# Performance work log

Hardware: AMD Instinct MI355X
Metric: run time of the kernel (lower is better)

Reference implementation:

```python
import jax, jax.numpy as jnp
import numpy as np

B, S = 4, 4096
DIM = 256
DF = 128   # dim_fourier = floor(256*0.5)
DS = 128   # dim_spline = 256 - 128
GF = 5     # fourier grid_size
GS = 5     # spline grid_size
K = 3      # spline order
P = 0.5
MIN_FREQ = 1e-6
LN_EPS = 1e-5


def _spline_grid():
    h = 2.0 / GS  # grid_range [-1, 1]
    g = np.arange(-K, GS + K + 1, dtype=np.float32) * h - 1.0
    return jnp.asarray(np.broadcast_to(g, (DS, g.shape[0])).copy())  # (DS, GS+2K+1)


def _base_freq():
    return jnp.asarray((1.0 / 10 ** np.linspace(0, 9, DF, dtype=np.float32)).reshape(DF, 1))


def b_splines(x, grid):
    # x: (N, DS); grid: (DS, GS+2K+1). Recursive de Boor B-spline basis.
    xe = x[:, :, None]
    bases = ((xe >= grid[:, :-1]) & (xe < grid[:, 1:])).astype(x.dtype)  # (N, DS, GS+2K)
    for k in range(1, K + 1):
        left = (xe - grid[:, : -(k + 1)]) / (grid[:, k:-1] - grid[:, : -(k + 1)])
        right = (grid[:, k + 1:] - xe) / (grid[:, k + 1:] - grid[:, 1:-k])
        bases = left * bases[:, :, :-1] + right * bases[:, :, 1:]
    return bases  # (N, DS, GS+K)


def setup_inputs() -> dict:
    key = jax.random.key(0)
    ks = jax.random.split(key, 8)
    timestamps = jax.random.uniform(ks[0], (B, S), dtype=jnp.float32)
    freq_theta = jnp.zeros((DF, 1), dtype=jnp.float32)
    bias_fourier = jnp.zeros((DF,), dtype=jnp.float32)
    fourier_weight = jax.random.normal(ks[1], (2, DF, DF, GF), dtype=jnp.float32) / (
        np.sqrt(DF) * np.sqrt(GF))
    w1_spline_w = jnp.asarray((1.0 / 10 ** np.linspace(0, 9, DS, dtype=np.float32)).reshape(DS, 1))
    w1_spline_b = jnp.zeros((DS,), dtype=jnp.float32)
    base_weight = jax.random.normal(ks[2], (DS, DS), dtype=jnp.float32) / np.sqrt(DS)
    spline_weight = jax.random.normal(ks[3], (DS, DS, GS + K), dtype=jnp.float32) / np.sqrt(DS * (GS + K))
    scale_weight = jnp.ones((DIM,), dtype=jnp.float32)
    ln_weight = jnp.ones((DIM,), dtype=jnp.float32)
    ln_bias = jnp.zeros((DIM,), dtype=jnp.float32)
    return {
        "timestamps": timestamps,
        "freq_theta": freq_theta,
        "bias_fourier": bias_fourier,
        "fourier_weight": fourier_weight,
        "w1_spline_w": w1_spline_w,
        "w1_spline_b": w1_spline_b,
        "base_weight": base_weight,
        "spline_weight": spline_weight,
        "scale_weight": scale_weight,
        "ln_weight": ln_weight,
        "ln_bias": ln_bias,
    }


def reference(timestamps, freq_theta, bias_fourier, fourier_weight,
              w1_spline_w, w1_spline_b, base_weight, spline_weight,
              scale_weight, ln_weight, ln_bias):
    grid = _spline_grid()
    base_freq = _base_freq()
    t = timestamps[..., None]  # (B, S, 1)

    # ---- Fourier branch ----
    freq_scale = jax.nn.softplus(freq_theta) + MIN_FREQ          # (DF, 1)
    freq_weight = base_freq * freq_scale                          # (DF, 1)
    proj_f = t * freq_weight[:, 0] + bias_fourier                 # (B, S, DF)
    xf = proj_f.reshape(-1, DF)                                   # (N, DF)
    kfreq = jnp.arange(1, GF + 1, dtype=xf.dtype)                 # (GF,)
    arg = xf[:, :, None] * kfreq                                  # (N, DF, GF)
    # Same math as torch's broadcast-then-sum, expressed as a contraction:
    # y[n,o] = sum_{d,g} cos(arg)[n,d,g] * Wc[o,d,g] + sin * Ws
    y_f = (jnp.einsum('ndg,odg->no', jnp.cos(arg), fourier_weight[0])
           + jnp.einsum('ndg,odg->no', jnp.sin(arg), fourier_weight[1])
           + fourier_weight[0].dtype.type(0) + jnp.zeros((DF,), xf.dtype))
    y_f = y_f  # bias of FourierSeries is zeros param; include explicitly below
    fourier_bias = jnp.zeros((DF,), xf.dtype)
    y_f = y_f + fourier_bias
    out_fourier = y_f.reshape(B, S, DF)

    # ---- Spline branch ----
    proj_s = t * w1_spline_w[:, 0] + w1_spline_b                  # (B, S, DS)
    xs = proj_s.reshape(-1, DS)                                   # (N, DS)
    base_out = jnp.tanh(xs) @ base_weight.T                       # (N, DS)
    bsp = b_splines(xs, grid).reshape(xs.shape[0], -1)            # (N, DS*(GS+K))
    spline_out = bsp @ spline_weight.reshape(DS, -1).T            # (N, DS)
    out_spline = (base_out + spline_out).reshape(B, S, DS)

    # ---- Combine (padded concat == concat of weighted halves) ----
    out = jnp.concatenate([out_fourier * P, out_spline * (1.0 - P)], axis=-1)  # (B, S, DIM)

    # LayerNorm then learnable scale
    mu = jnp.mean(out, axis=-1, keepdims=True)
    var = jnp.mean((out - mu) ** 2, axis=-1, keepdims=True)
    out = (out - mu) * jax.lax.rsqrt(var + LN_EPS) * ln_weight + ln_bias
    out = out * scale_weight
    return out
```

## Files before the change

kernel.cpp:

```cpp
#include <hip/hip_runtime.h>


typedef __attribute__((ext_vector_type(8))) _Float16 half8;
typedef __attribute__((ext_vector_type(2))) __fp16 fp16x2;
typedef __attribute__((ext_vector_type(16))) float f32x16;

#define KN5 -0.19999998807907104f
#define KN6  0.20000004768371582f
#define KN7  0.60000002384185791f

__device__ __forceinline__ unsigned pk(float a, float b) {
    fp16x2 h = __builtin_amdgcn_cvt_pkrtz(a, b);
    return __builtin_bit_cast(unsigned, h);
}

#define SPL9(x, o0,o1,o2,o3,o4,o5,o6,o7,o8) do {                          \
    float ax_ = fabsf(x);                                                  \
    float e_  = __expf(-2.f*ax_);                                          \
    float th_ = (1.f - e_) * __builtin_amdgcn_rcpf(1.f + e_);              \
    o0 = ((x) < 0.f) ? -th_ : th_;                                         \
    bool b1_ = ((x) >= KN6), b2_ = ((x) >= KN7);                           \
    float kn_ = b2_ ? KN7 : (b1_ ? KN6 : KN5);                             \
    float u_  = ((x) - kn_) * 2.5f;                                        \
    float um_ = 1.f - u_;                                                  \
    float u2_ = u_*u_, u3_ = u2_*u_, um2_ = um_*um_, um3_ = um2_*um_;      \
    float w0_ = (1.f/6.f)*um3_, w3_ = (1.f/6.f)*u3_;                       \
    float w1_ = 0.6666666666666667f - u2_  + 0.5f*u3_;                     \
    float w2_ = 0.6666666666666667f - um2_ + 0.5f*um3_;                    \
    o1 = 0.f; o2 = 0.f;                                                    \
    o3 = b1_ ? 0.f : w0_;                                                  \
    o4 = b2_ ? 0.f : (b1_ ? w0_ : w1_);                                    \
    o5 = b2_ ? w0_ : (b1_ ? w1_ : w2_);                                    \
    o6 = b2_ ? w1_ : (b1_ ? w2_ : w3_);                                    \
    o7 = b2_ ? w2_ : (b1_ ? w3_ : 0.f);                                    \
    o8 = b2_ ? w3_ : 0.f;                                                  \
} while (0)

__global__ __launch_bounds__(256) void prep_kernel(
    const float* __restrict__ FW,
    const float* __restrict__ BW,
    const float* __restrict__ SW,
    _Float16* __restrict__ WFP, _Float16* __restrict__ WSP)
{
    int tt = blockIdx.x * 256 + threadIdx.x;
    if (tt >= 327680) return;
    int e = tt & 7, l = (tt >> 3) & 63, frag = tt >> 9;
    int isS = frag >= 320;
    int f = isS ? frag - 320 : frag;
    int col = (f / 80) * 32 + (l & 31);
    int k = (f % 80) * 16 + (l >> 5) * 8 + e;
    int d = k / 10, j = k - d * 10;
    float val;
    if (!isS) {
        int p = (j >= 5), g = j - p * 5;
        val = FW[p * 81920 + col * 640 + d * 5 + g];
    } else {
        val = (j == 0) ? BW[col * 128 + d]
            : (j <= 8) ? SW[col * 1024 + d * 8 + (j - 1)] : 0.f;
    }
    (isS ? WSP : WFP)[(size_t)(f * 64 + l) * 8 + e] = (_Float16)val;
}

__global__ __launch_bounds__(256) void fused_kernel(
    const float* __restrict__ TS, const float* __restrict__ FTHETA,
    const float* __restrict__ BFOUR, const float* __restrict__ W1W,
    const float* __restrict__ W1B, const float* __restrict__ LNW,
    const float* __restrict__ LNB, const float* __restrict__ SCW,
    const _Float16* __restrict__ WFP, const _Float16* __restrict__ WSP,
    float* __restrict__ OUT)
{
    __shared__ __align__(16) _Float16 feat0[32 * 160];
    __shared__ __align__(16) _Float16 feat1[32 * 160];
    __shared__ float tsS[32], fwS[128], bfS[128], w1wS[128], w1bS[128];
    __shared__ float redS[32][4], redQ[32][4], muS[32], rsS[32];

    const int tid  = threadIdx.x;
    const int lane = tid & 63;
    const int wc   = tid >> 6;
    const int l31  = lane & 31, lh = lane >> 5;
    const int row0 = blockIdx.x * 32;

    if (tid < 32) tsS[tid] = TS[row0 + tid];
    if (tid < 128) {
        int d = tid;
        float th = FTHETA[d];
        float sp = (th > 20.f) ? th : log1pf(__expf(th));
        float ex = (float)((double)d * (9.0 / 127.0));
        fwS[d] = (1.0f / powf(10.f, ex)) * (sp + 1e-6f);
        bfS[d] = BFOUR[d];
    } else {
        int d = tid - 128;
        w1wS[d] = W1W[d];
        w1bS[d] = W1B[d];
    }
    __syncthreads();

    const int dd   = tid & 15;
    const int rowA = tid >> 4, rowB = rowA + 16;
    const float tA = tsS[rowA], tB = tsS[rowB];
    const int bA = rowA * 320 + dd * 20, swA = (rowA & 7) << 4;
    const int bB = rowB * 320 + dd * 20, swB = (rowB & 7) << 4;
    const int abase = l31 * 320, aswz = (l31 & 7) << 4;

    f32x16 acc1 = {};
    f32x16 acc2 = {};

    auto computeFour = [&](int ch, _Float16* buf) {
        int d = ch * 16 + dd;
        float fw = fwS[d], bf = bfS[d];
        char* p = (char*)buf;
#pragma unroll
        for (int q = 0; q < 2; ++q) {
            float base = (q ? tB : tA) * fw + bf;
            int b = q ? bB : bA, sw = q ? swB : swA;
            float s1, c1;
            __sincosf(base, &s1, &c1);
            float tc = c1 + c1;
            float c2 = tc*c1 - 1.f, c3 = tc*c2 - c1, c4 = tc*c3 - c2, c5 = tc*c4 - c3;
            float s2 = tc*s1,       s3 = tc*s2 - s1, s4 = tc*s3 - s2, s5 = tc*s4 - s3;
            *(unsigned*)(p + ((b +  0) ^ sw)) = pk(c1, c2);
            *(unsigned*)(p + ((b +  4) ^ sw)) = pk(c3, c4);
            *(unsigned*)(p + ((b +  8) ^ sw)) = pk(c5, s1);
            *(unsigned*)(p + ((b + 12) ^ sw)) = pk(s2, s3);
            *(unsigned*)(p + ((b + 16) ^ sw)) = pk(s4, s5);
        }
    };

    auto computeSpl = [&](int ch, _Float16* buf) {
        int d = ch * 16 + dd;
        float ww = w1wS[d], wb = w1bS[d];
        char* p = (char*)buf;
#pragma unroll
        for (int q = 0; q < 2; ++q) {
            float x = (q ? tB : tA) * ww + wb;
            int b = q ? bB : bA, sw = q ? swB : swA;
            float t0,b0,b1,b2,b3,b4,b5,b6,b7;
            SPL9(x, t0,b0,b1,b2,b3,b4,b5,b6,b7);
            *(unsigned*)(p + ((b +  0) ^ sw)) = pk(t0, b0);
            *(unsigned*)(p + ((b +  4) ^ sw)) = pk(b1, b2);
            *(unsigned*)(p + ((b +  8) ^ sw)) = pk(b3, b4);
            *(unsigned*)(p + ((b + 12) ^ sw)) = pk(b5, b6);
            *(unsigned*)(p + ((b + 16) ^ sw)) = pk(b7, 0.f);
        }
    };

    auto mfmaF = [&](int ch, const _Float16* buf) {
        const char* p = (const char*)buf;
#pragma unroll
        for (int ks = 0; ks < 10; ++ks) {
            half8 b = *(const half8*)(WFP + (size_t)((wc*80 + ch*10 + ks)*64 + lane) * 8);
            half8 a = *(const half8*)(p + ((abase + ks*32 + lh*16) ^ aswz));
            acc1 = __builtin_amdgcn_mfma_f32_32x32x16_f16(a, b, acc1, 0, 0, 0);
        }
    };

    auto mfmaS = [&](int ch, const _Float16* buf) {
        const char* p = (const char*)buf;
#pragma unroll
        for (int ks = 0; ks < 10; ++ks) {
            half8 b = *(const half8*)(WSP + (size_t)((wc*80 + ch*10 + ks)*64 + lane) * 8);
            half8 a = *(const half8*)(p + ((abase + ks*32 + lh*16) ^ aswz));
            acc2 = __builtin_amdgcn_mfma_f32_32x32x16_f16(a, b, acc2, 0, 0, 0);
        }
    };

    computeFour(0, feat0);
    __syncthreads();
    for (int ph = 0; ph < 16; ++ph) {
        _Float16* nb = ((ph + 1) & 1) ? feat1 : feat0;
        const _Float16* cb = (ph & 1) ? feat1 : feat0;
        int nx = ph + 1;
        if (nx < 8)       computeFour(nx, nb);
        else if (nx < 16) computeSpl(nx - 8, nb);
        if (ph < 8) mfmaF(ph, cb);
        else        mfmaS(ph - 8, cb);
        __syncthreads();
    }

#pragma unroll
    for (int g = 0; g < 16; ++g) {
        float xf = 0.5f * acc1[g];
        float xs = 0.5f * acc2[g];
        float s  = xf + xs;
        float qq = xf*xf + xs*xs;
#pragma unroll
        for (int m = 1; m < 32; m <<= 1) {
            s  += __shfl_xor(s, m);
            qq += __shfl_xor(qq, m);
        }
        if (l31 == 0) {
            int r = (g & 3) + 8*(g >> 2) + 4*lh;
            redS[r][wc] = s;
            redQ[r][wc] = qq;
        }
    }
    __syncthreads();
    if (tid < 32) {
        float s  = redS[tid][0] + redS[tid][1] + redS[tid][2] + redS[tid][3];
        float qq = redQ[tid][0] + redQ[tid][1] + redQ[tid][2] + redQ[tid][3];
        float mu = s * (1.0f / 256.0f);
        float var = qq * (1.0f / 256.0f) - mu * mu;
        muS[tid] = mu;
        rsS[tid] = rsqrtf(var + 1e-5f);
    }
    __syncthreads();
    {
        int cF = wc*32 + l31, cS = cF + 128;
        float gF = LNW[cF]*SCW[cF], hF = LNB[cF]*SCW[cF];
        float gS = LNW[cS]*SCW[cS], hS = LNB[cS]*SCW[cS];
#pragma unroll
        for (int g = 0; g < 16; ++g) {
            int r = (g & 3) + 8*(g >> 2) + 4*lh;
            float mu = muS[r], rr = rsS[r];
            size_t base = (size_t)(row0 + r) * 256;
            OUT[base + cF] = (0.5f*acc1[g] - mu)*rr*gF + hF;
            OUT[base + cS] = (0.5f*acc2[g] - mu)*rr*gS + hS;
        }
    }
}

extern "C" void kernel_launch(void* const* d_in, const int* in_sizes, int n_in,
                              void* d_out, int out_size, void* d_ws, size_t ws_size,
                              hipStream_t stream) {
    const float* TS     = (const float*)d_in[0];
    const float* FTHETA = (const float*)d_in[1];
    const float* BFOUR  = (const float*)d_in[2];
    const float* FW     = (const float*)d_in[3];
    const float* W1W    = (const float*)d_in[4];
    const float* W1B    = (const float*)d_in[5];
    const float* BW     = (const float*)d_in[6];
    const float* SW     = (const float*)d_in[7];
    const float* SCW    = (const float*)d_in[8];
    const float* LNW    = (const float*)d_in[9];
    const float* LNB    = (const float*)d_in[10];
    float* OUT = (float*)d_out;

    _Float16* WFP = (_Float16*)d_ws;
    _Float16* WSP = WFP + 163840;

    hipLaunchKernelGGL(prep_kernel, dim3(1280), dim3(256), 0, stream,
                       FW, BW, SW, WFP, WSP);
    hipLaunchKernelGGL(fused_kernel, dim3(512), dim3(256), 0, stream,
                       TS, FTHETA, BFOUR, W1W, W1B, LNW, LNB, SCW, WFP, WSP, OUT);
}
```

Before: 124.5 us.

## Split MFMA K dimension across two wave groups with 512-thread blocks

Doubles the block to 512 threads (8 waves) so that each feature-generation thread handles one row instead of two. The MFMA K loop is split across two wave halves, each doing 5 of the 10 k-steps, and the partial accumulators are combined through shared memory before the LayerNorm. The aim is more waves per block, hiding latency in the trig/spline feature generation and the MFMA chain, and shorter per-wave serial work. The cost is an extra shared-memory reduction pass, an added barrier, and possibly fewer blocks resident per CU.

```diff
diff --git a/kernel.cpp b/kernel.cpp
--- a/kernel.cpp
+++ b/kernel.cpp
@@ -61,7 +61,7 @@
     (isS ? WSP : WFP)[(size_t)(f * 64 + l) * 8 + e] = (_Float16)val;
 }
 
-__global__ __launch_bounds__(256) void fused_kernel(
+__global__ __launch_bounds__(512) void fused_kernel(
     const float* __restrict__ TS, const float* __restrict__ FTHETA,
     const float* __restrict__ BFOUR, const float* __restrict__ W1W,
     const float* __restrict__ W1B, const float* __restrict__ LNW,
@@ -69,98 +69,92 @@
     const _Float16* __restrict__ WFP, const _Float16* __restrict__ WSP,
     float* __restrict__ OUT)
 {
-    __shared__ __align__(16) _Float16 feat0[32 * 160];
-    __shared__ __align__(16) _Float16 feat1[32 * 160];
+    __shared__ __align__(16) char smem[32768];
     __shared__ float tsS[32], fwS[128], bfS[128], w1wS[128], w1bS[128];
-    __shared__ float redS[32][4], redQ[32][4], muS[32], rsS[32];
-
-    const int tid  = threadIdx.x;
-    const int lane = tid & 63;
-    const int wc   = tid >> 6;
-    const int l31  = lane & 31, lh = lane >> 5;
-    const int row0 = blockIdx.x * 32;
+    __shared__ float redS[32][8], redQ[32][8], muS[32], rsS[32];
+
+    const int tid   = threadIdx.x;
+    const int lane  = tid & 63;
+    const int w     = tid >> 6;
+    const int khalf = w >> 2, ct = w & 3;
+    const int l31   = lane & 31, lh = lane >> 5;
+    const int row0  = blockIdx.x * 32;
+
+    _Float16* feat0 = (_Float16*)smem;
+    _Float16* feat1 = (_Float16*)(smem + 10240);
 
     if (tid < 32) tsS[tid] = TS[row0 + tid];
-    if (tid < 128) {
-        int d = tid;
+    else if (tid >= 64 && tid < 192) {
+        int d = tid - 64;
         float th = FTHETA[d];
         float sp = (th > 20.f) ? th : log1pf(__expf(th));
         float ex = (float)((double)d * (9.0 / 127.0));
         fwS[d] = (1.0f / powf(10.f, ex)) * (sp + 1e-6f);
         bfS[d] = BFOUR[d];
-    } else {
-        int d = tid - 128;
+    } else if (tid >= 192 && tid < 320) {
+        int d = tid - 192;
         w1wS[d] = W1W[d];
         w1bS[d] = W1B[d];
     }
     __syncthreads();
 
     const int dd   = tid & 15;
-    const int rowA = tid >> 4, rowB = rowA + 16;
-    const float tA = tsS[rowA], tB = tsS[rowB];
-    const int bA = rowA * 320 + dd * 20, swA = (rowA & 7) << 4;
-    const int bB = rowB * 320 + dd * 20, swB = (rowB & 7) << 4;
+    const int frow = tid >> 4;
+    const float tF = tsS[frow];
+    const int bF = frow * 320 + dd * 20, swF = (frow & 7) << 4;
     const int abase = l31 * 320, aswz = (l31 & 7) << 4;
 
-    f32x16 acc1 = {};
-    f32x16 acc2 = {};
+    f32x16 accF = {};
+    f32x16 accS = {};
 
     auto computeFour = [&](int ch, _Float16* buf) {
         int d = ch * 16 + dd;
-        float fw = fwS[d], bf = bfS[d];
+        float base = tF * fwS[d] + bfS[d];
         char* p = (char*)buf;
-#pragma unroll
-        for (int q = 0; q < 2; ++q) {
-            float base = (q ? tB : tA) * fw + bf;
-            int b = q ? bB : bA, sw = q ? swB : swA;
-            float s1, c1;
-            __sincosf(base, &s1, &c1);
-            float tc = c1 + c1;
-            float c2 = tc*c1 - 1.f, c3 = tc*c2 - c1, c4 = tc*c3 - c2, c5 = tc*c4 - c3;
-            float s2 = tc*s1,       s3 = tc*s2 - s1, s4 = tc*s3 - s2, s5 = tc*s4 - s3;
-            *(unsigned*)(p + ((b +  0) ^ sw)) = pk(c1, c2);
-            *(unsigned*)(p + ((b +  4) ^ sw)) = pk(c3, c4);
-            *(unsigned*)(p + ((b +  8) ^ sw)) = pk(c5, s1);
-            *(unsigned*)(p + ((b + 12) ^ sw)) = pk(s2, s3);
-            *(unsigned*)(p + ((b + 16) ^ sw)) = pk(s4, s5);
-        }
+        float s1, c1;
+        __sincosf(base, &s1, &c1);
+        float tc = c1 + c1;
+        float c2 = tc*c1 - 1.f, c3 = tc*c2 - c1, c4 = tc*c3 - c2, c5 = tc*c4 - c3;
+        float s2 = tc*s1,       s3 = tc*s2 - s1, s4 = tc*s3 - s2, s5 = tc*s4 - s3;
+        *(unsigned*)(p + ((bF +  0) ^ swF)) = pk(c1, c2);
+        *(unsigned*)(p + ((bF +  4) ^ swF)) = pk(c3, c4);
+        *(unsigned*)(p + ((bF +  8) ^ swF)) = pk(c5, s1);
+        *(unsigned*)(p + ((bF + 12) ^ swF)) = pk(s2, s3);
+        *(unsigned*)(p + ((bF + 16) ^ swF)) = pk(s4, s5);
     };
 
     auto computeSpl = [&](int ch, _Float16* buf) {
         int d = ch * 16 + dd;
-        float ww = w1wS[d], wb = w1bS[d];
+        float x = tF * w1wS[d] + w1bS[d];
         char* p = (char*)buf;
-#pragma unroll
-        for (int q = 0; q < 2; ++q) {
-            float x = (q ? tB : tA) * ww + wb;
-            int b = q ? bB : bA, sw = q ? swB : swA;
-            float t0,b0,b1,b2,b3,b4,b5,b6,b7;
-            SPL9(x, t0,b0,b1,b2,b3,b4,b5,b6,b7);
-            *(unsigned*)(p + ((b +  0) ^ sw)) = pk(t0, b0);
-            *(unsigned*)(p + ((b +  4) ^ sw)) = pk(b1, b2);
-            *(unsigned*)(p + ((b +  8) ^ sw)) = pk(b3, b4);
-            *(unsigned*)(p + ((b + 12) ^ sw)) = pk(b5, b6);
-            *(unsigned*)(p + ((b + 16) ^ sw)) = pk(b7, 0.f);
-        }
+        float t0,b0,b1,b2,b3,b4,b5,b6,b7;
+        SPL9(x, t0,b0,b1,b2,b3,b4,b5,b6,b7);
+        *(unsigned*)(p + ((bF +  0) ^ swF)) = pk(t0, b0);
+        *(unsigned*)(p + ((bF +  4) ^ swF)) = pk(b1, b2);
+        *(unsigned*)(p + ((bF +  8) ^ swF)) = pk(b3, b4);
+        *(unsigned*)(p + ((bF + 12) ^ swF)) = pk(b5, b6);
+        *(unsigned*)(p + ((bF + 16) ^ swF)) = pk(b7, 0.f);
     };
 
     auto mfmaF = [&](int ch, const _Float16* buf) {
         const char* p = (const char*)buf;
 #pragma unroll
-        for (int ks = 0; ks < 10; ++ks) {
-            half8 b = *(const half8*)(WFP + (size_t)((wc*80 + ch*10 + ks)*64 + lane) * 8);
-            half8 a = *(const half8*)(p + ((abase + ks*32 + lh*16) ^ aswz));
-            acc1 = __builtin_amdgcn_mfma_f32_32x32x16_f16(a, b, acc1, 0, 0, 0);
+        for (int ks = 0; ks < 5; ++ks) {
+            int ksg = khalf * 5 + ks;
+            half8 b = *(const half8*)(WFP + (size_t)((ct*80 + ch*10 + ksg)*64 + lane) * 8);
+            half8 a = *(const half8*)(p + ((abase + ksg*32 + lh*16) ^ aswz));
+            accF = __builtin_amdgcn_mfma_f32_32x32x16_f16(a, b, accF, 0, 0, 0);
         }
     };
 
     auto mfmaS = [&](int ch, const _Float16* buf) {
         const char* p = (const char*)buf;
 #pragma unroll
-        for (int ks = 0; ks < 10; ++ks) {
-            half8 b = *(const half8*)(WSP + (size_t)((wc*80 + ch*10 + ks)*64 + lane) * 8);
-            half8 a = *(const half8*)(p + ((abase + ks*32 + lh*16) ^ aswz));
-            acc2 = __builtin_amdgcn_mfma_f32_32x32x16_f16(a, b, acc2, 0, 0, 0);
+        for (int ks = 0; ks < 5; ++ks) {
+            int ksg = khalf * 5 + ks;
+            half8 b = *(const half8*)(WSP + (size_t)((ct*80 + ch*10 + ksg)*64 + lane) * 8);
+            half8 a = *(const half8*)(p + ((abase + ksg*32 + lh*16) ^ aswz));
+            accS = __builtin_amdgcn_mfma_f32_32x32x16_f16(a, b, accS, 0, 0, 0);
         }
     };
 
@@ -177,12 +171,28 @@
         __syncthreads();
     }
 
+    float* part = (float*)smem;
 #pragma unroll
     for (int g = 0; g < 16; ++g) {
-        float xf = 0.5f * acc1[g];
-        float xs = 0.5f * acc2[g];
-        float s  = xf + xs;
-        float qq = xf*xf + xs*xs;
+        int r = (g & 3) + 8*(g >> 2) + 4*lh;
+        if (khalf) part[(ct    )*1024 + r*32 + l31] = accF[g];
+        else       part[(4 + ct)*1024 + r*32 + l31] = accS[g];
+    }
+    __syncthreads();
+    f32x16 fin;
+    const int colbase = khalf ? (128 + ct*32) : (ct*32);
+#pragma unroll
+    for (int g = 0; g < 16; ++g) {
+        int r = (g & 3) + 8*(g >> 2) + 4*lh;
+        float other = khalf ? part[(4 + ct)*1024 + r*32 + l31]
+                            : part[(ct    )*1024 + r*32 + l31];
+        fin[g] = 0.5f * ((khalf ? accS[g] : accF[g]) + other);
+    }
+
+#pragma unroll
+    for (int g = 0; g < 16; ++g) {
+        float s  = fin[g];
+        float qq = fin[g] * fin[g];
 #pragma unroll
         for (int m = 1; m < 32; m <<= 1) {
             s  += __shfl_xor(s, m);
@@ -190,14 +200,15 @@
         }
         if (l31 == 0) {
             int r = (g & 3) + 8*(g >> 2) + 4*lh;
-            redS[r][wc] = s;
-            redQ[r][wc] = qq;
+            redS[r][w] = s;
+            redQ[r][w] = qq;
         }
     }
     __syncthreads();
     if (tid < 32) {
-        float s  = redS[tid][0] + redS[tid][1] + redS[tid][2] + redS[tid][3];
-        float qq = redQ[tid][0] + redQ[tid][1] + redQ[tid][2] + redQ[tid][3];
+        float s = 0.f, qq = 0.f;
+#pragma unroll
+        for (int wv = 0; wv < 8; ++wv) { s += redS[tid][wv]; qq += redQ[tid][wv]; }
         float mu = s * (1.0f / 256.0f);
         float var = qq * (1.0f / 256.0f) - mu * mu;
         muS[tid] = mu;
@@ -205,16 +216,13 @@
     }
     __syncthreads();
     {
-        int cF = wc*32 + l31, cS = cF + 128;
-        float gF = LNW[cF]*SCW[cF], hF = LNB[cF]*SCW[cF];
-        float gS = LNW[cS]*SCW[cS], hS = LNB[cS]*SCW[cS];
+        int c = colbase + l31;
+        float gC = LNW[c] * SCW[c], hC = LNB[c] * SCW[c];
 #pragma unroll
         for (int g = 0; g < 16; ++g) {
             int r = (g & 3) + 8*(g >> 2) + 4*lh;
             float mu = muS[r], rr = rsS[r];
-            size_t base = (size_t)(row0 + r) * 256;
-            OUT[base + cF] = (0.5f*acc1[g] - mu)*rr*gF + hF;
-            OUT[base + cS] = (0.5f*acc2[g] - mu)*rr*gS + hS;
+            OUT[(size_t)(row0 + r) * 256 + c] = (fin[g] - mu) * rr * gC + hC;
         }
     }
 }
@@ -240,6 +248,6 @@
 
     hipLaunchKernelGGL(prep_kernel, dim3(1280), dim3(256), 0, stream,
                        FW, BW, SW, WFP, WSP);
-    hipLaunchKernelGGL(fused_kernel, dim3(512), dim3(256), 0, stream,
+    hipLaunchKernelGGL(fused_kernel, dim3(512), dim3(512), 0, stream,
                        TS, FTHETA, BFOUR, W1W, W1B, LNW, LNB, SCW, WFP, WSP, OUT);
 }
```

New measurement: 111.4 us. 1.12x faster.
